# Performance work log

Hardware: AMD Instinct MI355X
Metric: run time of the kernel (lower is better)

Reference implementation:

```python
import jax, jax.numpy as jnp
import numpy as np

H = 256      # hidden_dim
L = 3        # nb_layer
N = 10000    # nodes (shared between graph_1 and graph_2)
E1 = 131072  # edges in graph_1
E2 = 65536   # edges in graph_2
B = 16       # number of subgraphs / t_value batch


def _mlp(x, W0, b0, W1, b1, W2, b2):
    h = jax.nn.relu(x @ W0 + b0)
    h = jax.nn.relu(h @ W1 + b1)
    return h @ W2 + b2


def _gatv2(x, src, dst, e, Wl, bl, Wr, br, We, att, bias, n):
    # PyG GATv2Conv (heads=1): gather node features by edge, LeakyReLU attention
    # with edge encodings, scatter-softmax over destination nodes, scatter-add.
    xl = x @ Wl + bl                                            # (N, H)
    xr = x @ Wr + br                                            # (N, H)
    m = jax.nn.leaky_relu(xl[src] + xr[dst] + e @ We, 0.2)      # (E, H)
    logits = m @ att                                            # (E,)
    seg_max = jax.ops.segment_max(logits, dst, num_segments=n)
    ex = jnp.exp(logits - seg_max[dst])
    denom = jax.ops.segment_sum(ex, dst, num_segments=n)
    alpha = ex / (denom[dst] + 1e-16)                           # (E,)
    out = jax.ops.segment_sum(xl[src] * alpha[:, None], dst, num_segments=n)
    return out + bias


def _forward(edge_attr1, edge_attr2, t_value,
             te_W0, te_b0, te_W1, te_b1, te_W2, te_b2,
             ee_W0, ee_b0, ee_W1, ee_b1, ee_W2, ee_b2,
             dec_W0, dec_b0, dec_W1, dec_b1, dec_W2, dec_b2,
             gg_Wl, gg_bl, gg_Wr, gg_br, gg_We, gg_att, gg_bias,
             gf_Wl, gf_bl, gf_Wr, gf_br, gf_We, gf_att, gf_bias,
             edge_index1, edge_index2, batch):
    n = batch.shape[0]
    # time encoding per node, duplicated to 2H node features
    t_enc = _mlp(t_value[batch][:, None], te_W0, te_b0, te_W1, te_b1, te_W2, te_b2)  # (N, H)
    x = jnp.concatenate([t_enc, t_enc], axis=1)                                      # (N, 2H)
    e1 = _mlp(edge_attr1, ee_W0, ee_b0, ee_W1, ee_b1, ee_W2, ee_b2)                  # (E1, H)
    e2 = _mlp(edge_attr2[:, None], ee_W0, ee_b0, ee_W1, ee_b1, ee_W2, ee_b2)         # (E2, H)
    e1_init = e1
    src1, dst1 = edge_index1[0], edge_index1[1]
    src2, dst2 = edge_index2[0], edge_index2[1]
    for i in range(L):
        o1 = _gatv2(x, src1, dst1, e1, gg_Wl[i], gg_bl[i], gg_Wr[i], gg_br[i], gg_We[i], gg_att[i], gg_bias[i], n)
        o2 = _gatv2(x, src2, dst2, e2, gf_Wl[i], gf_bl[i], gf_Wr[i], gf_br[i], gf_We[i], gf_att[i], gf_bias[i], n)
        x = jnp.concatenate([o1, o2], axis=1)                                        # (N, 2H)
    # edge decoder: gather node pairs + initial edge encoding -> MLP
    dec_in = jnp.concatenate([x[src1], x[dst1], e1_init], axis=1)                    # (E1, 5H)
    return _mlp(dec_in, dec_W0, dec_b0, dec_W1, dec_b1, dec_W2, dec_b2)              # (E1, 1)


def setup_inputs() -> dict:
    ks = iter(jax.random.split(jax.random.key(0), 48))
    def nrm(shape, s=0.1):
        return jax.random.normal(next(ks), shape, dtype=jnp.float32) * s
    inp = {}
    inp["edge_index1"] = jax.random.randint(next(ks), (2, E1), 0, N)
    inp["edge_attr1"] = jax.random.uniform(next(ks), (E1, 1), dtype=jnp.float32)
    inp["edge_index2"] = jax.random.randint(next(ks), (2, E2), 0, N)
    inp["edge_attr2"] = jax.random.uniform(next(ks), (E2,), dtype=jnp.float32)
    inp["batch"] = jnp.sort(jax.random.randint(next(ks), (N,), 0, B))
    inp["t_value"] = jax.random.normal(next(ks), (B,), dtype=jnp.float32)
    for p in ["te", "ee"]:
        inp[p + "_W0"] = nrm((1, H)); inp[p + "_b0"] = jnp.zeros((H,), jnp.float32)
        inp[p + "_W1"] = nrm((H, H)); inp[p + "_b1"] = jnp.zeros((H,), jnp.float32)
        inp[p + "_W2"] = nrm((H, H)); inp[p + "_b2"] = jnp.zeros((H,), jnp.float32)
    inp["dec_W0"] = nrm((5 * H, H)); inp["dec_b0"] = jnp.zeros((H,), jnp.float32)
    inp["dec_W1"] = nrm((H, H));     inp["dec_b1"] = jnp.zeros((H,), jnp.float32)
    inp["dec_W2"] = nrm((H, 1));     inp["dec_b2"] = jnp.zeros((1,), jnp.float32)
    for p in ["gg", "gf"]:
        inp[p + "_Wl"] = nrm((L, 2 * H, H)); inp[p + "_bl"] = jnp.zeros((L, H), jnp.float32)
        inp[p + "_Wr"] = nrm((L, 2 * H, H)); inp[p + "_br"] = jnp.zeros((L, H), jnp.float32)
        inp[p + "_We"] = nrm((L, H, H))
        inp[p + "_att"] = nrm((L, H))
        inp[p + "_bias"] = jnp.zeros((L, H), jnp.float32)
    return inp


def reference(edge_index1, edge_attr1, edge_index2, edge_attr2, batch, t_value,
              te_W0, te_b0, te_W1, te_b1, te_W2, te_b2,
              ee_W0, ee_b0, ee_W1, ee_b1, ee_W2, ee_b2,
              dec_W0, dec_b0, dec_W1, dec_b1, dec_W2, dec_b2,
              gg_Wl, gg_bl, gg_Wr, gg_br, gg_We, gg_att, gg_bias,
              gf_Wl, gf_bl, gf_Wr, gf_br, gf_We, gf_att, gf_bias):
    return _forward(edge_attr1, edge_attr2, t_value,
                    te_W0, te_b0, te_W1, te_b1, te_W2, te_b2,
                    ee_W0, ee_b0, ee_W1, ee_b1, ee_W2, ee_b2,
                    dec_W0, dec_b0, dec_W1, dec_b1, dec_W2, dec_b2,
                    gg_Wl, gg_bl, gg_Wr, gg_br, gg_We, gg_att, gg_bias,
                    gf_Wl, gf_bl, gf_Wr, gf_br, gf_We, gf_att, gf_bias,
                    edge_index1, edge_index2, batch)
```

## Files before the change

kernel.cpp:

```cpp
#include <hip/hip_runtime.h>

#define Hd 256
#define NNODE 10000
#define NE1 131072
#define NE2 65536
#define TROWS 4097
#define TLD 1792

typedef __attribute__((ext_vector_type(8))) short bf16x8;
typedef __attribute__((ext_vector_type(4))) float f32x4;

#define MFMA16(a, b, c) __builtin_amdgcn_mfma_f32_16x16x32_bf16((a), (b), (c), 0, 0, 0)

__device__ __forceinline__ float b2f(ushort u) { return __uint_as_float(((unsigned)u) << 16); }
__device__ __forceinline__ ushort f2b(float f) {
  unsigned u = __float_as_uint(f);
  return (ushort)((u + 0x7fffu + ((u >> 16) & 1u)) >> 16);
}

__device__ __forceinline__ unsigned comb2(unsigned a, unsigned b, unsigned t) {
  float alo = __uint_as_float(a << 16), ahi = __uint_as_float(a & 0xffff0000u);
  float blo = __uint_as_float(b << 16), bhi = __uint_as_float(b & 0xffff0000u);
  float tlo = __uint_as_float(t << 16), thi = __uint_as_float(t & 0xffff0000u);
  float zlo = fmaxf(alo + blo + tlo, 0.f);
  float zhi = fmaxf(ahi + bhi + thi, 0.f);
  return ((unsigned)f2b(zhi) << 16) | (unsigned)f2b(zlo);
}


__global__ void time_mlp_k(const float* __restrict__ tval,
                           const float* __restrict__ W0, const float* __restrict__ b0,
                           const float* __restrict__ W1, const float* __restrict__ b1,
                           const float* __restrict__ W2, const float* __restrict__ b2,
                           float* __restrict__ tenc) {
  __shared__ float h0[Hd], h1[Hd];
  int b = blockIdx.x, j = threadIdx.x;
  float t = tval[b];
  h0[j] = fmaxf(t * W0[j] + b0[j], 0.f);
  __syncthreads();
  float a = b1[j];
  for (int k = 0; k < Hd; ++k) a += h0[k] * W1[k * Hd + j];
  h1[j] = fmaxf(a, 0.f);
  __syncthreads();
  float c = b2[j];
  for (int k = 0; k < Hd; ++k) c += h1[k] * W2[k * Hd + j];
  tenc[b * Hd + j] = c;
}

__global__ void build_x0_k(const int* __restrict__ batch, const float* __restrict__ tenc,
                           ushort* __restrict__ x0) {
  int idx = blockIdx.x * 256 + threadIdx.x;
  int n = idx >> 9;
  x0[idx] = f2b(tenc[batch[n] * Hd + (idx & 255)]);
}

__global__ void init_small_k(int* __restrict__ cnt1, int* __restrict__ cur1,
                             int* __restrict__ cnt2, int* __restrict__ cur2,
                             float* __restrict__ zerob, float* __restrict__ biascat,
                             const float* __restrict__ gg_bl, const float* __restrict__ gg_br,
                             const float* __restrict__ gf_bl, const float* __restrict__ gf_br) {
  int i = blockIdx.x * 256 + threadIdx.x;
  if (i < NNODE) { cnt1[i] = 0; cur1[i] = 0; cnt2[i] = 0; cur2[i] = 0; return; }
  i -= NNODE;
  if (i < 512) { zerob[i] = 0.f; return; }
  i -= 512;
  if (i < 6144) {
    int layer = i >> 10, c = i & 1023;
    float v;
    if (c < 256)      v = gg_bl[layer * 256 + c];
    else if (c < 512) v = gg_br[layer * 256 + c - 256];
    else if (c < 768) v = gf_bl[layer * 256 + c - 512];
    else              v = gf_br[layer * 256 + c - 768];
    biascat[layer * 1024 + c] = v;
  }
}

__global__ __launch_bounds__(256) void foldv2_k(
    const float* __restrict__ gg_We, const float* __restrict__ gf_We,
    const float* __restrict__ dec_W0, const float* __restrict__ eeW2,
    const float* __restrict__ eeb2,
    float* __restrict__ Wpart, float* __restrict__ bpart) {
  __shared__ float As[32][68];
  __shared__ float Bt[32][68];
  __shared__ float b2s[32];
  const int tid = threadIdx.x;
  const int bx = blockIdx.x, by = blockIdx.y, bz = blockIdx.z;
  const int y = bx >> 2, n0 = (bx & 3) * 64, k0 = by * 64;
  const int j0 = bz * 32;
  const bool by0 = (by == 0);
  const float* src;
  if (y < 6) src = ((y & 1) == 0 ? gg_We : gf_We) + (size_t)(y >> 1) * 65536;
  else       src = dec_W0 + 1024 * 256;
  if (tid < 32) b2s[tid] = eeb2[j0 + tid];
  {
    int nn = tid & 63, jj0 = tid >> 6;
#pragma unroll
    for (int p = 0; p < 8; ++p)
      As[jj0 + 4 * p][nn] = src[(size_t)(j0 + jj0 + 4 * p) * 256 + n0 + nn];
  }
  {
    int jj = tid & 31, kk0 = tid >> 5;
#pragma unroll
    for (int p = 0; p < 8; ++p)
      Bt[jj][kk0 + 8 * p] = eeW2[(size_t)(k0 + kk0 + 8 * p) * 256 + j0 + jj];
  }
  __syncthreads();
  const int tn = tid & 15, tk = tid >> 4;
  float acc[4][4];
#pragma unroll
  for (int a = 0; a < 4; ++a)
#pragma unroll
    for (int b = 0; b < 4; ++b) acc[a][b] = 0.f;
  float bacc[4] = {0.f, 0.f, 0.f, 0.f};
#pragma unroll 8
  for (int j = 0; j < 32; ++j) {
    float4 av = *(const float4*)&As[j][tn * 4];
    float4 bv = *(const float4*)&Bt[j][tk * 4];
    if (by0) {
      float eb = b2s[j];
      bacc[0] += eb * av.x; bacc[1] += eb * av.y;
      bacc[2] += eb * av.z; bacc[3] += eb * av.w;
    }
    acc[0][0] += av.x * bv.x; acc[0][1] += av.x * bv.y;
    acc[0][2] += av.x * bv.z; acc[0][3] += av.x * bv.w;
    acc[1][0] += av.y * bv.x; acc[1][1] += av.y * bv.y;
    acc[1][2] += av.y * bv.z; acc[1][3] += av.y * bv.w;
    acc[2][0] += av.z * bv.x; acc[2][1] += av.z * bv.y;
    acc[2][2] += av.z * bv.z; acc[2][3] += av.z * bv.w;
    acc[3][0] += av.w * bv.x; acc[3][1] += av.w * bv.y;
    acc[3][2] += av.w * bv.z; acc[3][3] += av.w * bv.w;
  }
  float* wp = Wpart + (size_t)bz * 458752;
#pragma unroll
  for (int a = 0; a < 4; ++a) {
    int n = n0 + tn * 4 + a;
#pragma unroll
    for (int b = 0; b < 4; ++b)
      wp[((size_t)y * 256 + n) * 256 + k0 + tk * 4 + b] = acc[a][b];
  }
  if (tk == 0 && by0) {
#pragma unroll
    for (int a = 0; a < 4; ++a)
      bpart[(size_t)bz * 1792 + y * 256 + n0 + tn * 4 + a] = bacc[a];
  }
}

__global__ __launch_bounds__(256) void foldr_k(
    const float* __restrict__ Wpart, const float* __restrict__ bpart,
    const float* __restrict__ dec_b0,
    ushort* __restrict__ WcatT, float* __restrict__ bcat) {
  int idx = blockIdx.x * 256 + threadIdx.x;
  float s = 0.f;
#pragma unroll
  for (int z = 0; z < 8; ++z) s += Wpart[(size_t)z * 458752 + idx];
  WcatT[idx] = f2b(s);
  if (idx < 1792) {
    float b = 0.f;
#pragma unroll
    for (int z = 0; z < 8; ++z) b += bpart[(size_t)z * 1792 + idx];
    if (idx >= 1536) b += dec_b0[idx - 1536];
    bcat[idx] = b;
  }
}

__global__ void build_h0_k(const float* __restrict__ W0, const float* __restrict__ b0,
                           ushort* __restrict__ h0b) {
  int i = blockIdx.x, j = threadIdx.x;
  float a = (float)i / 4096.f;
  h0b[(size_t)i * 256 + j] = f2b(fmaxf(a * W0[j] + b0[j], 0.f));
}

struct TT { const float* src; ushort* dst; int K; int n_off; int ld; int start; };
struct TransArgs { TT t[24]; };

__global__ void trans_all_k(TransArgs a) {
  int b = blockIdx.x;
  int ti = 0;
  while (ti + 1 < 24 && a.t[ti + 1].start <= b) ++ti;
  TT tk = a.t[ti];
  int lb = b - tk.start;
  int gx = tk.K >> 5;
  int k0 = (lb % gx) * 32, n0 = (lb / gx) * 32;
  __shared__ float t[32][33];
  int tx = threadIdx.x & 31, ty = threadIdx.x >> 5;
#pragma unroll
  for (int p = 0; p < 4; ++p)
    t[ty + 8 * p][tx] = tk.src[(size_t)(k0 + ty + 8 * p) * 256 + n0 + tx];
  __syncthreads();
#pragma unroll
  for (int p = 0; p < 4; ++p)
    tk.dst[(size_t)(tk.n_off + n0 + ty + 8 * p) * tk.ld + k0 + tx] = f2b(t[tx][ty + 8 * p]);
}


__global__ void deg_all_k(const int* __restrict__ dst1, int* __restrict__ cnt1,
                          const int* __restrict__ dst2, int* __restrict__ cnt2) {
  int e = blockIdx.x * 256 + threadIdx.x;
  if (e < NE1) atomicAdd(cnt1 + dst1[e], 1);
  else if (e - NE1 < NE2) atomicAdd(cnt2 + dst2[e - NE1], 1);
}

__global__ void scan_k(const int* __restrict__ cnt1, int* __restrict__ rs1,
                       const int* __restrict__ cnt2, int* __restrict__ rs2) {
  const int g = blockIdx.x;
  const int* cnt = g ? cnt2 : cnt1;
  int* rowstart = g ? rs2 : rs1;
  const int E = g ? NE2 : NE1;
  __shared__ int part[626];
  int t = threadIdx.x;
  if (t < 625) {
    int s = 0;
#pragma unroll
    for (int i = 0; i < 16; ++i) s += cnt[t * 16 + i];
    part[t] = s;
  }
  __syncthreads();
  if (t == 0) {
    int run = 0;
    for (int i = 0; i < 625; ++i) { int v = part[i]; part[i] = run; run += v; }
  }
  __syncthreads();
  if (t < 625) {
    int off = part[t];
#pragma unroll
    for (int i = 0; i < 16; ++i) { rowstart[t * 16 + i] = off; off += cnt[t * 16 + i]; }
  }
  if (t == 0) rowstart[NNODE] = E;
}

__global__ void fill_all_k(const int* __restrict__ dst1, const int* __restrict__ rs1,
                           int* __restrict__ cur1, int* __restrict__ eid1,
                           const int* __restrict__ src1, const float* __restrict__ eattr1,
                           int* __restrict__ srcs1, float* __restrict__ attrs1,
                           int* __restrict__ dsts1,
                           const int* __restrict__ dst2, const int* __restrict__ rs2,
                           int* __restrict__ cur2,
                           const int* __restrict__ src2, const float* __restrict__ eattr2,
                           int* __restrict__ srcs2, float* __restrict__ attrs2) {
  int e = blockIdx.x * 256 + threadIdx.x;
  if (e < NE1) {
    int d = dst1[e];
    int idx = rs1[d] + atomicAdd(cur1 + d, 1);
    eid1[idx] = e;
    srcs1[idx] = src1[e];
    attrs1[idx] = eattr1[e];
    dsts1[idx] = d;
  } else if (e - NE1 < NE2) {
    int e2 = e - NE1;
    int d = dst2[e2];
    int idx = rs2[d] + atomicAdd(cur2 + d, 1);
    srcs2[idx] = src2[e2];
    attrs2[idx] = eattr2[e2];
  }
}

__global__ __launch_bounds__(256) void attagg_k(
    const ushort* __restrict__ T, int tcol1, int tcol2,
    const float* __restrict__ att1, const float* __restrict__ att2,
    const ushort* __restrict__ xlr,
    const int* __restrict__ srcs1, const float* __restrict__ attrs1,
    const int* __restrict__ srcs2, const float* __restrict__ attrs2,
    const int* __restrict__ rs1, const int* __restrict__ rs2,
    const float* __restrict__ bias1, const float* __restrict__ bias2,
    ushort* __restrict__ xnext) {
  __shared__ float att_s[2][256], bias_s[2][256];
  __shared__ float acbuf[2][256];
  __shared__ float mden[2][2];
  const int tid = threadIdx.x;
  att_s[0][tid] = att1[tid];
  att_s[1][tid] = att2[tid];
  bias_s[0][tid] = bias1[tid];
  bias_s[1][tid] = bias2[tid];
  __syncthreads();
  const int wave = tid >> 6, lane = tid & 63;
  const int nloc = wave >> 1, sub = wave & 1;
  const bool g1 = blockIdx.x < (NNODE / 2);
  const int nid = (g1 ? blockIdx.x : blockIdx.x - NNODE / 2) * 2 + nloc;
  const int gi = g1 ? 0 : 1;
  const int* srcs = g1 ? srcs1 : srcs2;
  const float* attrs = g1 ? attrs1 : attrs2;
  const int* rowstart = g1 ? rs1 : rs2;
  const int goff = g1 ? 0 : 512;
  const int colbase = g1 ? 0 : 256;
  const ushort* Tg = T + (g1 ? tcol1 : tcol2);
  const int c = lane * 4;
  ushort4 xr4 = *(const ushort4*)(xlr + (size_t)nid * 1024 + goff + 256 + c);
  const float xr0 = b2f(xr4.x), xr1 = b2f(xr4.y), xr2 = b2f(xr4.z), xr3 = b2f(xr4.w);
  const float a0 = att_s[gi][c], a1 = att_s[gi][c + 1];
  const float a2 = att_s[gi][c + 2], a3 = att_s[gi][c + 3];
  const int s0 = rowstart[nid], s1 = rowstart[nid + 1];
  float m = -1e30f;
  float den = 0.f, ac0 = 0.f, ac1 = 0.f, ac2 = 0.f, ac3 = 0.f;
  {
    int i = s0 + sub;
    if (i < s1) {
      ushort4 xv0, lo0;
      ushort4 xv1 = {0, 0, 0, 0}, lo1 = {0, 0, 0, 0};
      {
        int s = srcs[i];
        int i0 = (int)(attrs[i] * 4096.f + 0.5f);
        i0 = i0 < 0 ? 0 : (i0 > 4096 ? 4096 : i0);
        lo0 = *(const ushort4*)(Tg + (size_t)i0 * TLD + c);
        xv0 = *(const ushort4*)(xlr + (size_t)s * 1024 + goff + c);
      }
      if (i + 2 < s1) {
        int s = srcs[i + 2];
        int i0 = (int)(attrs[i + 2] * 4096.f + 0.5f);
        i0 = i0 < 0 ? 0 : (i0 > 4096 ? 4096 : i0);
        lo1 = *(const ushort4*)(Tg + (size_t)i0 * TLD + c);
        xv1 = *(const ushort4*)(xlr + (size_t)s * 1024 + goff + c);
      }
      for (; i < s1; i += 2) {
        ushort4 xv_c = xv0, lo_c = lo0;
        xv0 = xv1; lo0 = lo1;
        if (i + 4 < s1) {
          int s = srcs[i + 4];
          int i0 = (int)(attrs[i + 4] * 4096.f + 0.5f);
          i0 = i0 < 0 ? 0 : (i0 > 4096 ? 4096 : i0);
          lo1 = *(const ushort4*)(Tg + (size_t)i0 * TLD + c);
          xv1 = *(const ushort4*)(xlr + (size_t)s * 1024 + goff + c);
        }
        float x0 = b2f(xv_c.x), x1 = b2f(xv_c.y), x2 = b2f(xv_c.z), x3 = b2f(xv_c.w);
        float z0 = x0 + xr0 + b2f(lo_c.x);
        float z1 = x1 + xr1 + b2f(lo_c.y);
        float z2 = x2 + xr2 + b2f(lo_c.z);
        float z3 = x3 + xr3 + b2f(lo_c.w);
        z0 = z0 > 0.f ? z0 : 0.2f * z0;
        z1 = z1 > 0.f ? z1 : 0.2f * z1;
        z2 = z2 > 0.f ? z2 : 0.2f * z2;
        z3 = z3 > 0.f ? z3 : 0.2f * z3;
        float p = z0 * a0 + z1 * a1 + z2 * a2 + z3 * a3;
#pragma unroll
        for (int dd = 1; dd < 64; dd <<= 1) p += __shfl_xor(p, dd);
        float mn = fmaxf(m, p);
        float sc = __expf(m - mn);
        float ww = __expf(p - mn);
        den = den * sc + ww;
        ac0 = ac0 * sc + ww * x0;
        ac1 = ac1 * sc + ww * x1;
        ac2 = ac2 * sc + ww * x2;
        ac3 = ac3 * sc + ww * x3;
        m = mn;
      }
    }
  }
  if (sub == 1) {
    acbuf[nloc][c + 0] = ac0;
    acbuf[nloc][c + 1] = ac1;
    acbuf[nloc][c + 2] = ac2;
    acbuf[nloc][c + 3] = ac3;
    if (lane == 0) { mden[nloc][0] = m; mden[nloc][1] = den; }
  }
  __syncthreads();
  if (sub == 0) {
    float m1 = mden[nloc][0], den1 = mden[nloc][1];
    float mn = fmaxf(m, m1);
    float sc0 = __expf(m - mn), sc1 = __expf(m1 - mn);
    float d = den * sc0 + den1 * sc1;
    float A0 = ac0 * sc0 + acbuf[nloc][c + 0] * sc1;
    float A1 = ac1 * sc0 + acbuf[nloc][c + 1] * sc1;
    float A2 = ac2 * sc0 + acbuf[nloc][c + 2] * sc1;
    float A3 = ac3 * sc0 + acbuf[nloc][c + 3] * sc1;
    float inv = 1.f / (d + 1e-16f);
    ushort4 o;
    o.x = f2b(A0 * inv + bias_s[gi][c + 0]);
    o.y = f2b(A1 * inv + bias_s[gi][c + 1]);
    o.z = f2b(A2 * inv + bias_s[gi][c + 2]);
    o.w = f2b(A3 * inv + bias_s[gi][c + 3]);
    *(ushort4*)(xnext + (size_t)nid * 512 + colbase + c) = o;
  }
}

template <bool RELU, bool OBF16>
__global__ __launch_bounds__(256, 3) void mgemm_k(
    const ushort* __restrict__ A, int lda, const ushort* __restrict__ WT, int K,
    const float* __restrict__ bias, void* __restrict__ C, int ldc, int M) {
  __shared__ ushort As[2][64][40];
  __shared__ ushort Bs[2][256][40];
  const int tid = threadIdx.x;
  const int wave = tid >> 6, lane = tid & 63;
  const int quad = lane >> 4, l15 = lane & 15;
  const int m0 = blockIdx.x * 64;
  const int ncol0 = blockIdx.y * 256;
  const ushort* WTb = WT + (size_t)ncol0 * K;
  const int arow = tid >> 2, akc = (tid & 3) << 3;
  int am = m0 + arow;
  if (am >= M) am = M - 1;
  const ushort* Arow = A + (size_t)am * lda + akc;
  const ushort* Brow = WTb + (size_t)arow * K + akc;
  f32x4 acc[4][4];
#pragma unroll
  for (int i = 0; i < 4; ++i)
#pragma unroll
    for (int j = 0; j < 4; ++j) acc[i][j] = (f32x4){0.f, 0.f, 0.f, 0.f};
  {
    uint4 ra = *(const uint4*)(Arow);
    uint4 rb0 = *(const uint4*)(Brow);
    uint4 rb1 = *(const uint4*)(Brow + (size_t)64 * K);
    uint4 rb2 = *(const uint4*)(Brow + (size_t)128 * K);
    uint4 rb3 = *(const uint4*)(Brow + (size_t)192 * K);
    *(uint4*)&As[0][arow][akc] = ra;
    *(uint4*)&Bs[0][arow][akc] = rb0;
    *(uint4*)&Bs[0][arow + 64][akc] = rb1;
    *(uint4*)&Bs[0][arow + 128][akc] = rb2;
    *(uint4*)&Bs[0][arow + 192][akc] = rb3;
  }
  __syncthreads();
  int cur = 0;
  for (int k0 = 0; k0 < K; k0 += 32) {
    const bool more = (k0 + 32 < K);
    uint4 ra, rb0, rb1, rb2, rb3;
    if (more) {
      ra = *(const uint4*)(Arow + k0 + 32);
      rb0 = *(const uint4*)(Brow + k0 + 32);
      rb1 = *(const uint4*)(Brow + (size_t)64 * K + k0 + 32);
      rb2 = *(const uint4*)(Brow + (size_t)128 * K + k0 + 32);
      rb3 = *(const uint4*)(Brow + (size_t)192 * K + k0 + 32);
    }
    bf16x8 bfr[4];
#pragma unroll
    for (int ni = 0; ni < 4; ++ni)
      bfr[ni] = *(const bf16x8*)&Bs[cur][wave * 64 + ni * 16 + l15][quad * 8];
#pragma unroll
    for (int mi = 0; mi < 4; ++mi) {
      bf16x8 af = *(const bf16x8*)&As[cur][mi * 16 + l15][quad * 8];
#pragma unroll
      for (int ni = 0; ni < 4; ++ni) acc[mi][ni] = MFMA16(af, bfr[ni], acc[mi][ni]);
    }
    if (more) {
      *(uint4*)&As[cur ^ 1][arow][akc] = ra;
      *(uint4*)&Bs[cur ^ 1][arow][akc] = rb0;
      *(uint4*)&Bs[cur ^ 1][arow + 64][akc] = rb1;
      *(uint4*)&Bs[cur ^ 1][arow + 128][akc] = rb2;
      *(uint4*)&Bs[cur ^ 1][arow + 192][akc] = rb3;
      __syncthreads();
    }
    cur ^= 1;
  }
#pragma unroll
  for (int mi = 0; mi < 4; ++mi)
#pragma unroll
    for (int ni = 0; ni < 4; ++ni) {
      int c = ncol0 + wave * 64 + ni * 16 + l15;
      float bv = bias[c];
#pragma unroll
      for (int r = 0; r < 4; ++r) {
        int m = m0 + mi * 16 + quad * 4 + r;
        if (m < M) {
          float v = acc[mi][ni][r] + bv;
          if (RELU) v = fmaxf(v, 0.f);
          if (OBF16) ((ushort*)C)[(size_t)m * ldc + c] = f2b(v);
          else       ((float*)C)[(size_t)m * ldc + c] = v;
        }
      }
    }
}

__global__ __launch_bounds__(256, 4) void dec3_k(
    const float* __restrict__ attrs1, const ushort* __restrict__ T,
    const ushort* __restrict__ Z, const int* __restrict__ eid,
    const int* __restrict__ srcs1, const int* __restrict__ dsts1,
    const ushort* __restrict__ W1T, const float* __restrict__ b1,
    const float* __restrict__ W2, const float* __restrict__ b2,
    float* __restrict__ out) {
  __shared__ __align__(16) ushort h0[64][264];
  float* red = (float*)h0;
  const int tid = threadIdx.x;
  const int wave = tid >> 6, lane = tid & 63;
  const int quad = lane >> 4, l15 = lane & 15;
  const int m0 = blockIdx.x * 64;
  const int arow = tid >> 2;
  {
    int gs = srcs1[m0 + arow], gd = dsts1[m0 + arow];
    int i0 = (int)(attrs1[m0 + arow] * 4096.f + 0.5f);
    i0 = i0 < 0 ? 0 : (i0 > 4096 ? 4096 : i0);
    const int cq = (tid & 3) * 8;
    const ushort* za = Z + (size_t)gs * 512 + cq;
    const ushort* zb = Z + (size_t)gd * 512 + 256 + cq;
    const ushort* tz = T + (size_t)i0 * TLD + 1536 + cq;
    uint4 ra[8], rb[8], rt[8];
#pragma unroll
    for (int s = 0; s < 8; ++s) ra[s] = *(const uint4*)(za + 32 * s);
#pragma unroll
    for (int s = 0; s < 8; ++s) rb[s] = *(const uint4*)(zb + 32 * s);
#pragma unroll
    for (int s = 0; s < 8; ++s) rt[s] = *(const uint4*)(tz + 32 * s);
    __builtin_amdgcn_sched_barrier(0);
#pragma unroll
    for (int s = 0; s < 8; ++s) {
      uint4 o;
      o.x = comb2(ra[s].x, rb[s].x, rt[s].x);
      o.y = comb2(ra[s].y, rb[s].y, rt[s].y);
      o.z = comb2(ra[s].z, rb[s].z, rt[s].z);
      o.w = comb2(ra[s].w, rb[s].w, rt[s].w);
      *(uint4*)&h0[arow][cq + 32 * s] = o;
    }
  }
  __syncthreads();
  f32x4 acc2[4][4];
#pragma unroll
  for (int i = 0; i < 4; ++i)
#pragma unroll
    for (int j = 0; j < 4; ++j) acc2[i][j] = (f32x4){0.f, 0.f, 0.f, 0.f};
  const ushort* wb = W1T + (size_t)(wave * 64 + l15) * 256 + quad * 8;
  bf16x8 bcur[4], bnxt[4];
#pragma unroll
  for (int ni = 0; ni < 4; ++ni)
    bcur[ni] = *(const bf16x8*)(wb + (size_t)(ni * 16) * 256);
#pragma unroll
  for (int k0 = 0; k0 < 256; k0 += 32) {
    if (k0 + 32 < 256) {
#pragma unroll
      for (int ni = 0; ni < 4; ++ni)
        bnxt[ni] = *(const bf16x8*)(wb + (size_t)(ni * 16) * 256 + k0 + 32);
    }
#pragma unroll
    for (int mi = 0; mi < 4; ++mi) {
      bf16x8 af = *(const bf16x8*)&h0[mi * 16 + l15][k0 + quad * 8];
#pragma unroll
      for (int ni = 0; ni < 4; ++ni) acc2[mi][ni] = MFMA16(af, bcur[ni], acc2[mi][ni]);
    }
#pragma unroll
    for (int ni = 0; ni < 4; ++ni) bcur[ni] = bnxt[ni];
  }
  float part[4][4];
#pragma unroll
  for (int mi = 0; mi < 4; ++mi)
#pragma unroll
    for (int r = 0; r < 4; ++r) part[mi][r] = 0.f;
#pragma unroll
  for (int mi = 0; mi < 4; ++mi)
#pragma unroll
    for (int ni = 0; ni < 4; ++ni) {
      int c = wave * 64 + ni * 16 + l15;
      float bv = b1[c], wv = W2[c];
#pragma unroll
      for (int r = 0; r < 4; ++r) {
        float v = fmaxf(acc2[mi][ni][r] + bv, 0.f);
        part[mi][r] += v * wv;
      }
    }
#pragma unroll
  for (int d = 1; d < 16; d <<= 1)
#pragma unroll
    for (int mi = 0; mi < 4; ++mi)
#pragma unroll
      for (int r = 0; r < 4; ++r) part[mi][r] += __shfl_xor(part[mi][r], d);
  __syncthreads();
  if (l15 == 0)
#pragma unroll
    for (int mi = 0; mi < 4; ++mi)
#pragma unroll
      for (int r = 0; r < 4; ++r) red[wave * 64 + mi * 16 + quad * 4 + r] = part[mi][r];
  __syncthreads();
  if (tid < 64) {
    float s = red[tid] + red[64 + tid] + red[128 + tid] + red[192 + tid];
    out[eid[m0 + tid]] = s + b2[0];
  }
}


extern "C" void kernel_launch(void* const* d_in, const int* in_sizes, int n_in,
                              void* d_out, int out_size, void* d_ws, size_t ws_size,
                              hipStream_t stream) {
  const int*   eidx1  = (const int*)d_in[0];
  const float* eattr1 = (const float*)d_in[1];
  const int*   eidx2  = (const int*)d_in[2];
  const float* eattr2 = (const float*)d_in[3];
  const int*   batch  = (const int*)d_in[4];
  const float* tval   = (const float*)d_in[5];
  const float* te_W0 = (const float*)d_in[6];
  const float* te_b0 = (const float*)d_in[7];
  const float* te_W1 = (const float*)d_in[8];
  const float* te_b1 = (const float*)d_in[9];
  const float* te_W2 = (const float*)d_in[10];
  const float* te_b2 = (const float*)d_in[11];
  const float* ee_W0 = (const float*)d_in[12];
  const float* ee_b0 = (const float*)d_in[13];
  const float* ee_W1 = (const float*)d_in[14];
  const float* ee_b1 = (const float*)d_in[15];
  const float* ee_W2 = (const float*)d_in[16];
  const float* ee_b2 = (const float*)d_in[17];
  const float* dec_W0 = (const float*)d_in[18];
  const float* dec_b0 = (const float*)d_in[19];
  const float* dec_W1 = (const float*)d_in[20];
  const float* dec_b1 = (const float*)d_in[21];
  const float* dec_W2 = (const float*)d_in[22];
  const float* dec_b2 = (const float*)d_in[23];
  const float* gg_Wl  = (const float*)d_in[24];
  const float* gg_bl  = (const float*)d_in[25];
  const float* gg_Wr  = (const float*)d_in[26];
  const float* gg_br  = (const float*)d_in[27];
  const float* gg_We  = (const float*)d_in[28];
  const float* gg_att = (const float*)d_in[29];
  const float* gg_bias= (const float*)d_in[30];
  const float* gf_Wl  = (const float*)d_in[31];
  const float* gf_bl  = (const float*)d_in[32];
  const float* gf_Wr  = (const float*)d_in[33];
  const float* gf_br  = (const float*)d_in[34];
  const float* gf_We  = (const float*)d_in[35];
  const float* gf_att = (const float*)d_in[36];
  const float* gf_bias= (const float*)d_in[37];
  (void)in_sizes; (void)n_in; (void)out_size; (void)ws_size;

  const int* src1 = eidx1;
  const int* dst1 = eidx1 + NE1;
  const int* src2 = eidx2;
  const int* dst2 = eidx2 + NE2;

  char* base = (char*)d_ws;
  size_t off = 0;
  auto alloc = [&](size_t bytes) {
    void* p = base + off;
    off += (bytes + 255) & ~(size_t)255;
    return p;
  };
  ushort* x_a    = (ushort*)alloc((size_t)NNODE * 512 * 2);
  ushort* x_b    = (ushort*)alloc((size_t)NNODE * 512 * 2);
  ushort* xlr    = (ushort*)alloc((size_t)NNODE * 1024 * 2);
  ushort* Z      = (ushort*)alloc((size_t)NNODE * 512 * 2);
  ushort* h0b    = (ushort*)alloc((size_t)TROWS * 256 * 2);
  ushort* H1     = (ushort*)alloc((size_t)TROWS * 256 * 2);
  ushort* T      = (ushort*)alloc((size_t)TROWS * TLD * 2);
  ushort* WcatT  = (ushort*)alloc((size_t)7 * 256 * 256 * 2);
  float*  bcat   = (float*)alloc((size_t)TLD * 4);
  float*  tenc   = (float*)alloc((size_t)16 * Hd * 4);
  ushort* decZT  = (ushort*)alloc((size_t)512 * 512 * 2);
  ushort* decW1T = (ushort*)alloc((size_t)256 * 256 * 2);
  ushort* eeW1T  = (ushort*)alloc((size_t)256 * 256 * 2);
  ushort* wlrT   = (ushort*)alloc((size_t)6 * 512 * 512 * 2);
  float*  biascat= (float*)alloc((size_t)6 * 1024 * 4);
  float*  zerob  = (float*)alloc((size_t)512 * 4);
  int* cnt1      = (int*)alloc((size_t)NNODE * 4);
  int* cur1      = (int*)alloc((size_t)NNODE * 4);
  int* rs1       = (int*)alloc((size_t)(NNODE + 1) * 4);
  int* eid1      = (int*)alloc((size_t)NE1 * 4);
  int* srcs1     = (int*)alloc((size_t)NE1 * 4);
  float* attrs1  = (float*)alloc((size_t)NE1 * 4);
  int* dsts1     = (int*)alloc((size_t)NE1 * 4);
  int* cnt2      = (int*)alloc((size_t)NNODE * 4);
  int* cur2      = (int*)alloc((size_t)NNODE * 4);
  int* rs2       = (int*)alloc((size_t)(NNODE + 1) * 4);
  int* srcs2     = (int*)alloc((size_t)NE2 * 4);
  float* attrs2  = (float*)alloc((size_t)NE2 * 4);

  float* Wpart = (float*)T;
  float* bpart = (float*)H1;

  float* out = (float*)d_out;

  init_small_k<<<(NNODE + 512 + 6144 + 255) / 256, 256, 0, stream>>>(
      cnt1, cur1, cnt2, cur2, zerob, biascat, gg_bl, gg_br, gf_bl, gf_br);
  foldv2_k<<<dim3(28, 4, 8), 256, 0, stream>>>(gg_We, gf_We, dec_W0, ee_W2, ee_b2,
                                               Wpart, bpart);
  foldr_k<<<1792, 256, 0, stream>>>(Wpart, bpart, dec_b0, WcatT, bcat);
  build_h0_k<<<TROWS, 256, 0, stream>>>(ee_W0, ee_b0, h0b);

  TransArgs ta;
  int nt = 0, cum = 0;
  auto add = [&](const float* s, ushort* d, int K, int noff, int ld) {
    ta.t[nt].src = s; ta.t[nt].dst = d; ta.t[nt].K = K;
    ta.t[nt].n_off = noff; ta.t[nt].ld = ld; ta.t[nt].start = cum;
    cum += (K / 32) * 8; ++nt;
  };
  add(dec_W1, decW1T, 256, 0, 256);
  add(ee_W1, eeW1T, 256, 0, 256);
  add(dec_W0, decZT, 512, 0, 512);
  add(dec_W0 + 512 * 256, decZT, 512, 256, 512);
  for (int i = 0; i < 3; ++i) {
    add(gg_Wl + (size_t)i * 512 * 256, wlrT + (size_t)(2 * i) * 512 * 512, 512, 0, 512);
    add(gg_Wr + (size_t)i * 512 * 256, wlrT + (size_t)(2 * i) * 512 * 512, 512, 256, 512);
    add(gf_Wl + (size_t)i * 512 * 256, wlrT + (size_t)(2 * i + 1) * 512 * 512, 512, 0, 512);
    add(gf_Wr + (size_t)i * 512 * 256, wlrT + (size_t)(2 * i + 1) * 512 * 512, 512, 256, 512);
  }
  for (int i = nt; i < 24; ++i) ta.t[i].start = 0x7fffffff;
  trans_all_k<<<cum, 256, 0, stream>>>(ta);

  mgemm_k<true, true><<<dim3((TROWS + 63) / 64, 1), 256, 0, stream>>>(
      h0b, 256, eeW1T, 256, ee_b1, H1, 256, TROWS);
  mgemm_k<false, true><<<dim3((TROWS + 63) / 64, 7), 256, 0, stream>>>(
      H1, 256, WcatT, 256, bcat, T, TLD, TROWS);

  deg_all_k<<<(NE1 + NE2) / 256, 256, 0, stream>>>(dst1, cnt1, dst2, cnt2);
  scan_k<<<2, 640, 0, stream>>>(cnt1, rs1, cnt2, rs2);
  fill_all_k<<<(NE1 + NE2) / 256, 256, 0, stream>>>(
      dst1, rs1, cur1, eid1, src1, eattr1, srcs1, attrs1, dsts1,
      dst2, rs2, cur2, src2, eattr2, srcs2, attrs2);

  time_mlp_k<<<16, 256, 0, stream>>>(tval, te_W0, te_b0, te_W1, te_b1, te_W2, te_b2, tenc);
  build_x0_k<<<(NNODE * 512) / 256, 256, 0, stream>>>(batch, tenc, x_a);

  ushort* x_cur = x_a;
  ushort* x_nxt = x_b;
  const int ngrid = (NNODE + 63) / 64;
  for (int i = 0; i < 3; ++i) {
    mgemm_k<false, true><<<dim3(ngrid, 4), 256, 0, stream>>>(
        x_cur, 512, wlrT + (size_t)(2 * i) * 512 * 512, 512, biascat + (size_t)i * 1024, xlr, 1024, NNODE);
    attagg_k<<<NNODE, 256, 0, stream>>>(
        T, (2 * i) * 256, (2 * i + 1) * 256,
        gg_att + i * Hd, gf_att + i * Hd, xlr,
        srcs1, attrs1, srcs2, attrs2, rs1, rs2,
        gg_bias + i * Hd, gf_bias + i * Hd, x_nxt);
    ushort* t = x_cur; x_cur = x_nxt; x_nxt = t;
  }

  mgemm_k<false, true><<<dim3(ngrid, 2), 256, 0, stream>>>(
      x_cur, 512, decZT, 512, zerob, Z, 512, NNODE);
  dec3_k<<<NE1 / 64, 256, 0, stream>>>(attrs1, T, Z, eid1, srcs1, dsts1,
                                       decW1T, dec_b1, dec_W2, dec_b2, out);
}
```

Measured before the change: 491.1 us.

## Use direct global-to-LDS loads in GEMM and precompute packed edge offsets

The GEMM kernel now loads tiles straight from global memory into LDS with global_load_lds. That removes the register staging, the padding on the LDS rows, and one of the conditional syncs, and the occupancy hint is raised from 3 to 4. Edge records are packed into int2 pairs holding the source row offset and the quantized attribute table offset, computed once in the fill kernel. This removes the repeated float-to-index conversion and halves the index loads in the attention and decoder kernels. Dropping the LDS padding may add bank conflicts on the MFMA fragment reads, and the direct-to-LDS addressing depends on the per-lane layout matching what the hardware writes.

```diff
diff --git a/kernel.cpp b/kernel.cpp
--- a/kernel.cpp
+++ b/kernel.cpp
@@ -16,6 +16,12 @@
 __device__ __forceinline__ ushort f2b(float f) {
   unsigned u = __float_as_uint(f);
   return (ushort)((u + 0x7fffu + ((u >> 16) & 1u)) >> 16);
+}
+
+__device__ __forceinline__ void gload16(const ushort* g, ushort* l) {
+  __builtin_amdgcn_global_load_lds(
+      (const __attribute__((address_space(1))) unsigned int*)g,
+      (__attribute__((address_space(3))) unsigned int*)l, 16, 0, 0);
 }
 
 __device__ __forceinline__ unsigned comb2(unsigned a, unsigned b, unsigned t) {
@@ -231,26 +237,27 @@
 __global__ void fill_all_k(const int* __restrict__ dst1, const int* __restrict__ rs1,
                            int* __restrict__ cur1, int* __restrict__ eid1,
                            const int* __restrict__ src1, const float* __restrict__ eattr1,
-                           int* __restrict__ srcs1, float* __restrict__ attrs1,
-                           int* __restrict__ dsts1,
+                           int2* __restrict__ es1, int* __restrict__ dsts1,
                            const int* __restrict__ dst2, const int* __restrict__ rs2,
                            int* __restrict__ cur2,
                            const int* __restrict__ src2, const float* __restrict__ eattr2,
-                           int* __restrict__ srcs2, float* __restrict__ attrs2) {
+                           int2* __restrict__ es2) {
   int e = blockIdx.x * 256 + threadIdx.x;
   if (e < NE1) {
     int d = dst1[e];
     int idx = rs1[d] + atomicAdd(cur1 + d, 1);
     eid1[idx] = e;
-    srcs1[idx] = src1[e];
-    attrs1[idx] = eattr1[e];
+    int i0 = (int)(eattr1[e] * 4096.f + 0.5f);
+    i0 = i0 < 0 ? 0 : (i0 > 4096 ? 4096 : i0);
+    es1[idx] = make_int2(src1[e] * 1024, i0 * TLD);
     dsts1[idx] = d;
   } else if (e - NE1 < NE2) {
     int e2 = e - NE1;
     int d = dst2[e2];
     int idx = rs2[d] + atomicAdd(cur2 + d, 1);
-    srcs2[idx] = src2[e2];
-    attrs2[idx] = eattr2[e2];
+    int i0 = (int)(eattr2[e2] * 4096.f + 0.5f);
+    i0 = i0 < 0 ? 0 : (i0 > 4096 ? 4096 : i0);
+    es2[idx] = make_int2(src2[e2] * 1024, i0 * TLD);
   }
 }
 
@@ -258,8 +265,7 @@
     const ushort* __restrict__ T, int tcol1, int tcol2,
     const float* __restrict__ att1, const float* __restrict__ att2,
     const ushort* __restrict__ xlr,
-    const int* __restrict__ srcs1, const float* __restrict__ attrs1,
-    const int* __restrict__ srcs2, const float* __restrict__ attrs2,
+    const int2* __restrict__ es1, const int2* __restrict__ es2,
     const int* __restrict__ rs1, const int* __restrict__ rs2,
     const float* __restrict__ bias1, const float* __restrict__ bias2,
     ushort* __restrict__ xnext) {
@@ -277,8 +283,7 @@
   const bool g1 = blockIdx.x < (NNODE / 2);
   const int nid = (g1 ? blockIdx.x : blockIdx.x - NNODE / 2) * 2 + nloc;
   const int gi = g1 ? 0 : 1;
-  const int* srcs = g1 ? srcs1 : srcs2;
-  const float* attrs = g1 ? attrs1 : attrs2;
+  const int2* es = g1 ? es1 : es2;
   const int* rowstart = g1 ? rs1 : rs2;
   const int goff = g1 ? 0 : 512;
   const int colbase = g1 ? 0 : 256;
@@ -297,28 +302,22 @@
       ushort4 xv0, lo0;
       ushort4 xv1 = {0, 0, 0, 0}, lo1 = {0, 0, 0, 0};
       {
-        int s = srcs[i];
-        int i0 = (int)(attrs[i] * 4096.f + 0.5f);
-        i0 = i0 < 0 ? 0 : (i0 > 4096 ? 4096 : i0);
-        lo0 = *(const ushort4*)(Tg + (size_t)i0 * TLD + c);
-        xv0 = *(const ushort4*)(xlr + (size_t)s * 1024 + goff + c);
+        int2 e0 = es[i];
+        lo0 = *(const ushort4*)(Tg + e0.y + c);
+        xv0 = *(const ushort4*)(xlr + e0.x + goff + c);
       }
       if (i + 2 < s1) {
-        int s = srcs[i + 2];
-        int i0 = (int)(attrs[i + 2] * 4096.f + 0.5f);
-        i0 = i0 < 0 ? 0 : (i0 > 4096 ? 4096 : i0);
-        lo1 = *(const ushort4*)(Tg + (size_t)i0 * TLD + c);
-        xv1 = *(const ushort4*)(xlr + (size_t)s * 1024 + goff + c);
+        int2 e1 = es[i + 2];
+        lo1 = *(const ushort4*)(Tg + e1.y + c);
+        xv1 = *(const ushort4*)(xlr + e1.x + goff + c);
       }
       for (; i < s1; i += 2) {
         ushort4 xv_c = xv0, lo_c = lo0;
         xv0 = xv1; lo0 = lo1;
         if (i + 4 < s1) {
-          int s = srcs[i + 4];
-          int i0 = (int)(attrs[i + 4] * 4096.f + 0.5f);
-          i0 = i0 < 0 ? 0 : (i0 > 4096 ? 4096 : i0);
-          lo1 = *(const ushort4*)(Tg + (size_t)i0 * TLD + c);
-          xv1 = *(const ushort4*)(xlr + (size_t)s * 1024 + goff + c);
+          int2 en = es[i + 4];
+          lo1 = *(const ushort4*)(Tg + en.y + c);
+          xv1 = *(const ushort4*)(xlr + en.x + goff + c);
         }
         float x0 = b2f(xv_c.x), x1 = b2f(xv_c.y), x2 = b2f(xv_c.z), x3 = b2f(xv_c.w);
         float z0 = x0 + xr0 + b2f(lo_c.x);
@@ -372,11 +371,11 @@
 }
 
 template <bool RELU, bool OBF16>
-__global__ __launch_bounds__(256, 3) void mgemm_k(
+__global__ __launch_bounds__(256, 4) void mgemm_k(
     const ushort* __restrict__ A, int lda, const ushort* __restrict__ WT, int K,
     const float* __restrict__ bias, void* __restrict__ C, int ldc, int M) {
-  __shared__ ushort As[2][64][40];
-  __shared__ ushort Bs[2][256][40];
+  __shared__ ushort As[2][64][32];
+  __shared__ ushort Bs[2][256][32];
   const int tid = threadIdx.x;
   const int wave = tid >> 6, lane = tid & 63;
   const int quad = lane >> 4, l15 = lane & 15;
@@ -393,29 +392,18 @@
   for (int i = 0; i < 4; ++i)
 #pragma unroll
     for (int j = 0; j < 4; ++j) acc[i][j] = (f32x4){0.f, 0.f, 0.f, 0.f};
-  {
-    uint4 ra = *(const uint4*)(Arow);
-    uint4 rb0 = *(const uint4*)(Brow);
-    uint4 rb1 = *(const uint4*)(Brow + (size_t)64 * K);
-    uint4 rb2 = *(const uint4*)(Brow + (size_t)128 * K);
-    uint4 rb3 = *(const uint4*)(Brow + (size_t)192 * K);
-    *(uint4*)&As[0][arow][akc] = ra;
-    *(uint4*)&Bs[0][arow][akc] = rb0;
-    *(uint4*)&Bs[0][arow + 64][akc] = rb1;
-    *(uint4*)&Bs[0][arow + 128][akc] = rb2;
-    *(uint4*)&Bs[0][arow + 192][akc] = rb3;
-  }
+  gload16(Arow, &As[0][arow][akc]);
+#pragma unroll
+  for (int r = 0; r < 4; ++r)
+    gload16(Brow + (size_t)(r * 64) * K, &Bs[0][arow + r * 64][akc]);
   __syncthreads();
   int cur = 0;
   for (int k0 = 0; k0 < K; k0 += 32) {
-    const bool more = (k0 + 32 < K);
-    uint4 ra, rb0, rb1, rb2, rb3;
-    if (more) {
-      ra = *(const uint4*)(Arow + k0 + 32);
-      rb0 = *(const uint4*)(Brow + k0 + 32);
-      rb1 = *(const uint4*)(Brow + (size_t)64 * K + k0 + 32);
-      rb2 = *(const uint4*)(Brow + (size_t)128 * K + k0 + 32);
-      rb3 = *(const uint4*)(Brow + (size_t)192 * K + k0 + 32);
+    if (k0 + 32 < K) {
+      gload16(Arow + k0 + 32, &As[cur ^ 1][arow][akc]);
+#pragma unroll
+      for (int r = 0; r < 4; ++r)
+        gload16(Brow + (size_t)(r * 64) * K + k0 + 32, &Bs[cur ^ 1][arow + r * 64][akc]);
     }
     bf16x8 bfr[4];
 #pragma unroll
@@ -427,14 +415,7 @@
 #pragma unroll
       for (int ni = 0; ni < 4; ++ni) acc[mi][ni] = MFMA16(af, bfr[ni], acc[mi][ni]);
     }
-    if (more) {
-      *(uint4*)&As[cur ^ 1][arow][akc] = ra;
-      *(uint4*)&Bs[cur ^ 1][arow][akc] = rb0;
-      *(uint4*)&Bs[cur ^ 1][arow + 64][akc] = rb1;
-      *(uint4*)&Bs[cur ^ 1][arow + 128][akc] = rb2;
-      *(uint4*)&Bs[cur ^ 1][arow + 192][akc] = rb3;
-      __syncthreads();
-    }
+    __syncthreads();
     cur ^= 1;
   }
 #pragma unroll
@@ -457,9 +438,9 @@
 }
 
 __global__ __launch_bounds__(256, 4) void dec3_k(
-    const float* __restrict__ attrs1, const ushort* __restrict__ T,
+    const int2* __restrict__ es1, const ushort* __restrict__ T,
     const ushort* __restrict__ Z, const int* __restrict__ eid,
-    const int* __restrict__ srcs1, const int* __restrict__ dsts1,
+    const int* __restrict__ dsts1,
     const ushort* __restrict__ W1T, const float* __restrict__ b1,
     const float* __restrict__ W2, const float* __restrict__ b2,
     float* __restrict__ out) {
@@ -471,13 +452,12 @@
   const int m0 = blockIdx.x * 64;
   const int arow = tid >> 2;
   {
-    int gs = srcs1[m0 + arow], gd = dsts1[m0 + arow];
-    int i0 = (int)(attrs1[m0 + arow] * 4096.f + 0.5f);
-    i0 = i0 < 0 ? 0 : (i0 > 4096 ? 4096 : i0);
+    int2 ee = es1[m0 + arow];
+    int gd = dsts1[m0 + arow];
     const int cq = (tid & 3) * 8;
-    const ushort* za = Z + (size_t)gs * 512 + cq;
+    const ushort* za = Z + (ee.x >> 1) + cq;
     const ushort* zb = Z + (size_t)gd * 512 + 256 + cq;
-    const ushort* tz = T + (size_t)i0 * TLD + 1536 + cq;
+    const ushort* tz = T + ee.y + 1536 + cq;
     uint4 ra[8], rb[8], rt[8];
 #pragma unroll
     for (int s = 0; s < 8; ++s) ra[s] = *(const uint4*)(za + 32 * s);
@@ -635,14 +615,12 @@
   int* cur1      = (int*)alloc((size_t)NNODE * 4);
   int* rs1       = (int*)alloc((size_t)(NNODE + 1) * 4);
   int* eid1      = (int*)alloc((size_t)NE1 * 4);
-  int* srcs1     = (int*)alloc((size_t)NE1 * 4);
-  float* attrs1  = (float*)alloc((size_t)NE1 * 4);
+  int2* es1      = (int2*)alloc((size_t)NE1 * 8);
   int* dsts1     = (int*)alloc((size_t)NE1 * 4);
   int* cnt2      = (int*)alloc((size_t)NNODE * 4);
   int* cur2      = (int*)alloc((size_t)NNODE * 4);
   int* rs2       = (int*)alloc((size_t)(NNODE + 1) * 4);
-  int* srcs2     = (int*)alloc((size_t)NE2 * 4);
-  float* attrs2  = (float*)alloc((size_t)NE2 * 4);
+  int2* es2      = (int2*)alloc((size_t)NE2 * 8);
 
   float* Wpart = (float*)T;
   float* bpart = (float*)H1;
@@ -684,8 +662,8 @@
   deg_all_k<<<(NE1 + NE2) / 256, 256, 0, stream>>>(dst1, cnt1, dst2, cnt2);
   scan_k<<<2, 640, 0, stream>>>(cnt1, rs1, cnt2, rs2);
   fill_all_k<<<(NE1 + NE2) / 256, 256, 0, stream>>>(
-      dst1, rs1, cur1, eid1, src1, eattr1, srcs1, attrs1, dsts1,
-      dst2, rs2, cur2, src2, eattr2, srcs2, attrs2);
+      dst1, rs1, cur1, eid1, src1, eattr1, es1, dsts1,
+      dst2, rs2, cur2, src2, eattr2, es2);
 
   time_mlp_k<<<16, 256, 0, stream>>>(tval, te_W0, te_b0, te_W1, te_b1, te_W2, te_b2, tenc);
   build_x0_k<<<(NNODE * 512) / 256, 256, 0, stream>>>(batch, tenc, x_a);
@@ -699,13 +677,13 @@
     attagg_k<<<NNODE, 256, 0, stream>>>(
         T, (2 * i) * 256, (2 * i + 1) * 256,
         gg_att + i * Hd, gf_att + i * Hd, xlr,
-        srcs1, attrs1, srcs2, attrs2, rs1, rs2,
+        es1, es2, rs1, rs2,
         gg_bias + i * Hd, gf_bias + i * Hd, x_nxt);
     ushort* t = x_cur; x_cur = x_nxt; x_nxt = t;
   }
 
   mgemm_k<false, true><<<dim3(ngrid, 2), 256, 0, stream>>>(
       x_cur, 512, decZT, 512, zerob, Z, 512, NNODE);
-  dec3_k<<<NE1 / 64, 256, 0, stream>>>(attrs1, T, Z, eid1, srcs1, dsts1,
+  dec3_k<<<NE1 / 64, 256, 0, stream>>>(es1, T, Z, eid1, dsts1,
                                        decW1T, dec_b1, dec_W2, dec_b2, out);
 }
```

New measurement: 490.1 us. No clear change (-0.2%).
